# Kernel tuning notes

Hardware: AMD Instinct MI355X
Metric: run time of the kernel (lower is better)

Reference implementation:

```python
import jax, jax.numpy as jnp
import numpy as np

B, C, H, W = 8, 256, 64, 64
IC = 128  # inter_channels = C // reduction


def setup_inputs() -> dict:
    key = jax.random.key(0)
    ks = jax.random.split(key, 9)
    s_in = 1.0 / np.sqrt(C)
    s_ic = 1.0 / np.sqrt(IC)
    return {
        "x": jax.random.normal(ks[0], (B, C, H, W), jnp.float32),
        "wg": jax.random.normal(ks[1], (IC, C), jnp.float32) * s_in,
        "bg": jax.random.normal(ks[2], (IC,), jnp.float32) * s_in,
        "wt": jax.random.normal(ks[3], (IC, C), jnp.float32) * s_in,
        "bt": jax.random.normal(ks[4], (IC,), jnp.float32) * s_in,
        "wp": jax.random.normal(ks[5], (IC, C), jnp.float32) * s_in,
        "bp": jax.random.normal(ks[6], (IC,), jnp.float32) * s_in,
        "wm": jax.random.normal(ks[7], (C, IC), jnp.float32) * s_ic,
        "bm": jax.random.normal(ks[8], (C,), jnp.float32) * s_ic,
    }


def reference(x, wg, bg, wt, bt, wp, bp, wm, bm):
    b, c, h, w = x.shape
    n = h * w
    xf = x.reshape(b, c, n)  # [B, C, N]
    # 1x1 convs are channel matmuls; relu applied after each (as in source)
    g = jax.nn.relu(jnp.einsum('ic,bcn->bni', wg, xf) + bg)          # [B, N, IC]
    theta = jax.nn.relu(jnp.einsum('ic,bcn->bni', wt, xf) + bt)      # [B, N, IC]
    phi = jax.nn.relu(jnp.einsum('ic,bcn->bin', wp, xf) + bp[:, None])  # [B, IC, N]
    scores = jnp.einsum('bni,bim->bnm', theta, phi)                  # [B, N, N] (no scaling)
    attn = jax.nn.softmax(scores, axis=-1)
    out = jnp.einsum('bnm,bmi->bni', attn, g)                        # [B, N, IC]
    mask = jax.nn.relu(jnp.einsum('oc,bnc->bon', wm, out) + bm[None, :, None])
    return mask.reshape(b, c, h, w) + x
```

## Files before the change

kernel.cpp:

```cpp
#include <hip/hip_runtime.h>

typedef __bf16 bf16x8 __attribute__((ext_vector_type(8)));
typedef float f32x4 __attribute__((ext_vector_type(4)));
typedef float f32x16 __attribute__((ext_vector_type(16)));
typedef unsigned short ushort8 __attribute__((ext_vector_type(8)));
typedef unsigned short ushort4v __attribute__((ext_vector_type(4)));
typedef unsigned int uint4v __attribute__((ext_vector_type(4)));

union Frag {
  ushort8 u;
  bf16x8 b;
  uint4v w;
};

__device__ __forceinline__ unsigned short f2bf(float f) {
  unsigned int u = __float_as_uint(f);
  u += 0x7fffu + ((u >> 16) & 1u);
  return (unsigned short)(u >> 16);
}

__device__ __forceinline__ f32x4 fz4() {
  f32x4 v; v[0] = 0.f; v[1] = 0.f; v[2] = 0.f; v[3] = 0.f; return v;
}

__device__ __forceinline__ f32x16 fz16() {
  f32x16 v;
#pragma unroll
  for (int i = 0; i < 16; ++i) v[i] = 0.f;
  return v;
}

#define MFMA16(a, b, c) __builtin_amdgcn_mfma_f32_16x16x32_bf16(a, b, c, 0, 0, 0)
#define MFMA32(a, b, c) __builtin_amdgcn_mfma_f32_32x32x16_bf16(a, b, c, 0, 0, 0)


__global__ void k_prep(const float* __restrict__ wg, const float* __restrict__ wt,
                       const float* __restrict__ wp, const float* __restrict__ wm,
                       unsigned short* __restrict__ wcat, unsigned short* __restrict__ wmb) {
  int t = blockIdx.x * 256 + threadIdx.x;
  if (t < 98304) {
    int o = t >> 8;
    const float* src = (o < 128) ? wt : ((o < 256) ? wp : wg);
    wcat[t] = f2bf(src[(o & 127) * 256 + (t & 255)]);
  }
  if (t < 32768) wmb[t] = f2bf(wm[t]);
}

__device__ __forceinline__ void stage_x(const float* __restrict__ x, int bx, int pt0,
                                        unsigned short* xb, int tid) {
  int c0 = (tid >> 2) * 4;
  int psub = (tid & 3) * 16;
  const float* xbase = x + (size_t)bx * 256 * 4096 + pt0;
  for (int ppc = 0; ppc < 4; ++ppc) {
    int p0 = psub + ppc * 4;
    f32x4 r0 = *(const f32x4*)(xbase + (size_t)(c0 + 0) * 4096 + p0);
    f32x4 r1 = *(const f32x4*)(xbase + (size_t)(c0 + 1) * 4096 + p0);
    f32x4 r2 = *(const f32x4*)(xbase + (size_t)(c0 + 2) * 4096 + p0);
    f32x4 r3 = *(const f32x4*)(xbase + (size_t)(c0 + 3) * 4096 + p0);
    for (int e = 0; e < 4; ++e) {
      ushort4v wv;
      wv[0] = f2bf(r0[e]); wv[1] = f2bf(r1[e]); wv[2] = f2bf(r2[e]); wv[3] = f2bf(r3[e]);
      *(ushort4v*)&xb[(p0 + e) * 264 + c0] = wv;
    }
  }
}

__global__ __launch_bounds__(256, 2) void k_proj_tp(
    const float* __restrict__ x, const unsigned short* __restrict__ wcat,
    const float* __restrict__ bt, const float* __restrict__ bp,
    unsigned short* __restrict__ theta, unsigned short* __restrict__ phiS) {
  __shared__ unsigned short xb[64 * 264];
  int gb = blockIdx.x >> 6;
  size_t ob_off = (size_t)gb * 524288;
  int pt0 = (blockIdx.x & 63) << 6;
  int tid = threadIdx.x;
  stage_x(x, gb, pt0, xb, tid);
  __syncthreads();
  int l = tid & 63, w = tid >> 6, lr = l & 15, lg = l >> 4;
  int obase = w * 64;
  f32x4 acc[4][4];
  for (int i = 0; i < 4; ++i) for (int j = 0; j < 4; ++j) acc[i][j] = fz4();
  for (int kc = 0; kc < 8; ++kc) {
    int ko = kc * 32 + 8 * lg;
    Frag wa[4], xq[4];
    for (int ot = 0; ot < 4; ++ot)
      wa[ot].u = *(const ushort8*)(wcat + (size_t)(obase + ot * 16 + lr) * 256 + ko);
    for (int pt = 0; pt < 4; ++pt)
      xq[pt].u = *(const ushort8*)&xb[(pt * 16 + lr) * 264 + ko];
    for (int ot = 0; ot < 4; ++ot)
      for (int pt = 0; pt < 4; ++pt)
        acc[ot][pt] = MFMA16(wa[ot].b, xq[pt].b, acc[ot][pt]);
  }
  for (int ot = 0; ot < 4; ++ot) {
    int o0 = obase + ot * 16 + 4 * lg;
    float bias[4];
    for (int j = 0; j < 4; ++j) bias[j] = (o0 < 128) ? bt[o0 + j] : bp[o0 + j - 128];
    for (int pt = 0; pt < 4; ++pt) {
      int n = pt0 + pt * 16 + lr;
      ushort4v wv;
      for (int j = 0; j < 4; ++j) {
        float v = acc[ot][pt][j] + bias[j];
        wv[j] = f2bf(v > 0.f ? v : 0.f);
      }
      if (o0 < 128) {
        *(ushort4v*)(theta + ob_off + (size_t)n * 128 + o0) = wv;
      } else {
        int oc = o0 - 128;
        size_t a = (size_t)(n >> 5) * 4096 + (size_t)(oc >> 4) * 512 +
                   (size_t)((oc >> 3) & 1) * 256 + (size_t)(n & 31) * 8 + (oc & 7);
        *(ushort4v*)(phiS + ob_off + a) = wv;
      }
    }
  }
}

__global__ __launch_bounds__(256, 2) void k_proj_g(
    const float* __restrict__ x, const unsigned short* __restrict__ wcat,
    const float* __restrict__ bg, unsigned short* __restrict__ vS) {
  __shared__ unsigned short xb[64 * 264];
  int gb = blockIdx.x >> 6;
  size_t ob_off = (size_t)gb * 524288;
  int pt0 = (blockIdx.x & 63) << 6;
  int tid = threadIdx.x;
  stage_x(x, gb, pt0, xb, tid);
  __syncthreads();
  int l = tid & 63, w = tid >> 6, lr = l & 15, lg = l >> 4;
  f32x4 acc[8];
  for (int i = 0; i < 8; ++i) acc[i] = fz4();
  for (int kc = 0; kc < 8; ++kc) {
    int ko = kc * 32 + 8 * lg;
    Frag xa;
    xa.u = *(const ushort8*)&xb[(w * 16 + lr) * 264 + ko];
    for (int ot = 0; ot < 8; ++ot) {
      Frag wb;
      wb.u = *(const ushort8*)(wcat + (size_t)(256 + ot * 16 + lr) * 256 + ko);
      acc[ot] = MFMA16(xa.b, wb.b, acc[ot]);
    }
  }
  for (int ot = 0; ot < 8; ++ot) {
    int o = ot * 16 + lr;
    float bias = bg[o];
    int n0 = pt0 + w * 16 + 4 * lg;
    ushort4v wv;
    for (int j = 0; j < 4; ++j) {
      float v = acc[ot][j] + bias;
      wv[j] = f2bf(v > 0.f ? v : 0.f);
    }
    size_t a = (size_t)(n0 >> 5) * 4096 +
               (size_t)((o >> 5) * 2 + ((n0 >> 4) & 1)) * 512 +
               (size_t)((((n0 >> 3) & 1) << 5) | (o & 31)) * 8 + (n0 & 7);
    *(ushort4v*)(vS + ob_off + a) = wv;
  }
}

__global__ __launch_bounds__(256, 2) void k_attn(
    const unsigned short* __restrict__ theta, const unsigned short* __restrict__ phiS,
    const unsigned short* __restrict__ vS, unsigned short* __restrict__ out_nm) {
  __shared__ float osum[32][132];
  __shared__ float mls[4][32][2];
  int bid = blockIdx.x;
  int b = bid & 7;
  int q0 = (bid >> 3) << 5;
  int tid = threadIdx.x;
  int l = tid & 63, wid = tid >> 6;
  int ml = l & 31, hi = l >> 5;
  int l8 = l * 8;

  const size_t tbase = ((size_t)b << 12) * 128;
  const unsigned short* pS = phiS + (size_t)b * 524288;
  const unsigned short* vSb = vS + (size_t)b * 524288;

  Frag qf[8];
#pragma unroll
  for (int kc = 0; kc < 8; ++kc)
    qf[kc].u = *(const ushort8*)(theta + tbase +
        (size_t)(q0 + ml) * 128 + kc * 16 + 8 * hi);

  f32x16 oacc[4];
#pragma unroll
  for (int db = 0; db < 4; ++db) oacc[db] = fz16();
  float m = -1e30f, sden = 0.f;

  int t0 = wid * 32;
  Frag pa[8], vt[8];

#pragma unroll
  for (int kc = 0; kc < 8; ++kc)
    pa[kc].u = *(const ushort8*)(pS + (size_t)t0 * 4096 + kc * 512 + l8);

  for (int kt = 0; kt < 32; ++kt) {
    int t = t0 + kt;

    f32x16 sacc = fz16();
#pragma unroll
    for (int kc = 0; kc < 8; ++kc) sacc = MFMA32(pa[kc].b, qf[kc].b, sacc);

#pragma unroll
    for (int t8 = 0; t8 < 8; ++t8)
      vt[t8].u = *(const ushort8*)(vSb + (size_t)t * 4096 + t8 * 512 + l8);

    int tn = t0 + ((kt + 1) & 31);
#pragma unroll
    for (int kc = 0; kc < 8; ++kc)
      pa[kc].u = *(const ushort8*)(pS + (size_t)tn * 4096 + kc * 512 + l8);

    float p[16];
#pragma unroll
    for (int r = 0; r < 16; ++r) p[r] = sacc[r];
    float m8[8];
#pragma unroll
    for (int j = 0; j < 8; ++j) m8[j] = fmaxf(p[j], p[j + 8]);
    float mt = fmaxf(fmaxf(fmaxf(m8[0], m8[1]), fmaxf(m8[2], m8[3])),
                     fmaxf(fmaxf(m8[4], m8[5]), fmaxf(m8[6], m8[7])));
    mt = fmaxf(mt, __shfl_xor(mt, 32));
    if (!__all(mt <= m + 8.0f)) {
      float mn = fmaxf(m, mt);
      float sc = __expf(m - mn);
      sden *= sc;
#pragma unroll
      for (int db = 0; db < 4; ++db) oacc[db] *= sc;
      m = mn;
    }
#pragma unroll
    for (int r = 0; r < 16; ++r) p[r] = __expf(p[r] - m);
    float s8[8];
#pragma unroll
    for (int j = 0; j < 8; ++j) s8[j] = p[j] + p[j + 8];
    float ps = ((s8[0] + s8[1]) + (s8[2] + s8[3])) + ((s8[4] + s8[5]) + (s8[6] + s8[7]));
    ps += __shfl_xor(ps, 32);
    sden += ps;

    unsigned wpk[8], pw[8];
#pragma unroll
    for (int j = 0; j < 8; ++j)
      wpk[j] = (unsigned)f2bf(p[2 * j]) | ((unsigned)f2bf(p[2 * j + 1]) << 16);
#pragma unroll
    for (int j = 0; j < 8; ++j) pw[j] = (unsigned)__shfl_xor((int)wpk[j], 32);
    Frag bf0, bf1;
    bf0.w[0] = hi ? pw[2] : wpk[0];
    bf0.w[1] = hi ? pw[3] : wpk[1];
    bf0.w[2] = hi ? wpk[2] : pw[0];
    bf0.w[3] = hi ? wpk[3] : pw[1];
    bf1.w[0] = hi ? pw[6] : wpk[4];
    bf1.w[1] = hi ? pw[7] : wpk[5];
    bf1.w[2] = hi ? wpk[6] : pw[4];
    bf1.w[3] = hi ? wpk[7] : pw[5];

#pragma unroll
    for (int db = 0; db < 4; ++db) {
      oacc[db] = MFMA32(vt[db * 2].b, bf0.b, oacc[db]);
      oacc[db] = MFMA32(vt[db * 2 + 1].b, bf1.b, oacc[db]);
    }
  }

  if (l < 32) { mls[wid][l][0] = m; mls[wid][l][1] = sden; }
  __syncthreads();
  float M = fmaxf(fmaxf(mls[0][ml][0], mls[1][ml][0]),
                  fmaxf(mls[2][ml][0], mls[3][ml][0]));
  float sc = __expf(m - M);
  for (int w = 0; w < 4; ++w) {
    if (wid == w) {
#pragma unroll
      for (int db = 0; db < 4; ++db)
#pragma unroll
        for (int r = 0; r < 16; ++r) {
          int d = db * 32 + (r & 3) + 8 * (r >> 2) + 4 * hi;
          if (w == 0) osum[ml][d] = oacc[db][r] * sc;
          else        osum[ml][d] += oacc[db][r] * sc;
        }
    }
    __syncthreads();
  }
  {
    int row = wid * 8 + (l >> 3);
    int d0 = (l & 7) * 16;
    float Mx = fmaxf(fmaxf(mls[0][row][0], mls[1][row][0]),
                     fmaxf(mls[2][row][0], mls[3][row][0]));
    float Lt = 0.f;
    for (int w = 0; w < 4; ++w) Lt += mls[w][row][1] * __expf(mls[w][row][0] - Mx);
    float inv = 1.0f / Lt;
    ushort8 w1;
    for (int k = 0; k < 8; ++k) w1[k] = f2bf(osum[row][d0 + k] * inv);
    ushort8 w2;
    for (int k = 0; k < 8; ++k) w2[k] = f2bf(osum[row][d0 + 8 + k] * inv);
    size_t base = tbase + (size_t)(q0 + row) * 128 + d0;
    *(ushort8*)(out_nm + base) = w1;
    *(ushort8*)(out_nm + base + 8) = w2;
  }
}

__global__ __launch_bounds__(256, 2) void k_mask(
    const unsigned short* __restrict__ wmb, const unsigned short* __restrict__ out_nm,
    const float* __restrict__ bm, const float* __restrict__ x,
    float* __restrict__ out) {
  int gb = blockIdx.x >> 6;
  size_t boff = (size_t)gb * 524288;
  int n0 = (blockIdx.x & 63) << 6;
  int tid = threadIdx.x;
  int l = tid & 63, w = tid >> 6, lr = l & 15, lg = l >> 4;
  int ob = w * 64;
  f32x4 acc[4][4];
  for (int i = 0; i < 4; ++i) for (int j = 0; j < 4; ++j) acc[i][j] = fz4();
  for (int kc = 0; kc < 4; ++kc) {
    int ko = kc * 32 + 8 * lg;
    Frag wa[4], xq[4];
    for (int ot = 0; ot < 4; ++ot)
      wa[ot].u = *(const ushort8*)(wmb + (size_t)(ob + ot * 16 + lr) * 128 + ko);
    for (int nt = 0; nt < 4; ++nt)
      xq[nt].u = *(const ushort8*)(out_nm + boff + (size_t)(n0 + nt * 16 + lr) * 128 + ko);
    for (int ot = 0; ot < 4; ++ot)
      for (int nt = 0; nt < 4; ++nt)
        acc[ot][nt] = MFMA16(wa[ot].b, xq[nt].b, acc[ot][nt]);
  }
  for (int ot = 0; ot < 4; ++ot) {
    int o0 = ob + ot * 16 + 4 * lg;
    for (int nt = 0; nt < 4; ++nt) {
      int n = n0 + nt * 16 + lr;
      for (int j = 0; j < 4; ++j) {
        size_t idx = ((size_t)(gb << 8) + o0 + j) * 4096 + n;
        float v = acc[ot][nt][j] + bm[o0 + j];
        v = v > 0.f ? v : 0.f;
        out[idx] = v + x[idx];
      }
    }
  }
}

extern "C" void kernel_launch(void* const* d_in, const int* in_sizes, int n_in,
                              void* d_out, int out_size, void* d_ws, size_t ws_size,
                              hipStream_t stream) {
  const float* x  = (const float*)d_in[0];
  const float* wg = (const float*)d_in[1];
  const float* bg = (const float*)d_in[2];
  const float* wt = (const float*)d_in[3];
  const float* bt = (const float*)d_in[4];
  const float* wp = (const float*)d_in[5];
  const float* bp = (const float*)d_in[6];
  const float* wm = (const float*)d_in[7];
  const float* bm = (const float*)d_in[8];
  float* out = (float*)d_out;

  const size_t SLAB = 524288;
  unsigned short* wcat  = (unsigned short*)d_ws;
  unsigned short* wmb   = wcat + 98304;
  unsigned short* theta = wmb + 32768;
  unsigned short* phiS  = theta + 8 * SLAB;
  unsigned short* vS    = phiS + 8 * SLAB;

  k_prep<<<384, 256, 0, stream>>>(wg, wt, wp, wm, wcat, wmb);
  k_proj_tp<<<512, 256, 0, stream>>>(x, wcat, bt, bp, theta, phiS);
  k_proj_g<<<512, 256, 0, stream>>>(x, wcat, bg, vS);
  k_attn<<<1024, 256, 0, stream>>>(theta, phiS, vS, theta );
  k_mask<<<512, 256, 0, stream>>>(wmb, theta, bm, x, out);
}
```

Measured before the change: 163.7 us.

## Fuse projections, use exp2 softmax, setprio around MFMAs, swizzle attention output

```diff
diff --git a/kernel.cpp b/kernel.cpp
--- a/kernel.cpp
+++ b/kernel.cpp
@@ -32,6 +32,8 @@
 
 #define MFMA16(a, b, c) __builtin_amdgcn_mfma_f32_16x16x32_bf16(a, b, c, 0, 0, 0)
 #define MFMA32(a, b, c) __builtin_amdgcn_mfma_f32_32x32x16_bf16(a, b, c, 0, 0, 0)
+
+#define LOG2E 1.4426950408889634f
 
 
 __global__ void k_prep(const float* __restrict__ wg, const float* __restrict__ wt,
@@ -65,10 +67,12 @@
   }
 }
 
-__global__ __launch_bounds__(256, 2) void k_proj_tp(
+__global__ __launch_bounds__(256, 2) void k_proj(
     const float* __restrict__ x, const unsigned short* __restrict__ wcat,
     const float* __restrict__ bt, const float* __restrict__ bp,
-    unsigned short* __restrict__ theta, unsigned short* __restrict__ phiS) {
+    const float* __restrict__ bg,
+    unsigned short* __restrict__ theta, unsigned short* __restrict__ phiS,
+    unsigned short* __restrict__ vS) {
   __shared__ unsigned short xb[64 * 264];
   int gb = blockIdx.x >> 6;
   size_t ob_off = (size_t)gb * 524288;
@@ -79,7 +83,9 @@
   int l = tid & 63, w = tid >> 6, lr = l & 15, lg = l >> 4;
   int obase = w * 64;
   f32x4 acc[4][4];
+  f32x4 accg[8];
   for (int i = 0; i < 4; ++i) for (int j = 0; j < 4; ++j) acc[i][j] = fz4();
+  for (int i = 0; i < 8; ++i) accg[i] = fz4();
   for (int kc = 0; kc < 8; ++kc) {
     int ko = kc * 32 + 8 * lg;
     Frag wa[4], xq[4];
@@ -90,6 +96,11 @@
     for (int ot = 0; ot < 4; ++ot)
       for (int pt = 0; pt < 4; ++pt)
         acc[ot][pt] = MFMA16(wa[ot].b, xq[pt].b, acc[ot][pt]);
+    for (int ot = 0; ot < 8; ++ot) {
+      Frag wb;
+      wb.u = *(const ushort8*)(wcat + (size_t)(256 + ot * 16 + lr) * 256 + ko);
+      accg[ot] = MFMA16(xq[w].b, wb.b, accg[ot]);
+    }
   }
   for (int ot = 0; ot < 4; ++ot) {
     int o0 = obase + ot * 16 + 4 * lg;
@@ -98,43 +109,22 @@
     for (int pt = 0; pt < 4; ++pt) {
       int n = pt0 + pt * 16 + lr;
       ushort4v wv;
-      for (int j = 0; j < 4; ++j) {
-        float v = acc[ot][pt][j] + bias[j];
-        wv[j] = f2bf(v > 0.f ? v : 0.f);
-      }
       if (o0 < 128) {
+        for (int j = 0; j < 4; ++j) {
+          float v = acc[ot][pt][j] + bias[j];
+          wv[j] = f2bf(v > 0.f ? v * LOG2E : 0.f);
+        }
         *(ushort4v*)(theta + ob_off + (size_t)n * 128 + o0) = wv;
       } else {
+        for (int j = 0; j < 4; ++j) {
+          float v = acc[ot][pt][j] + bias[j];
+          wv[j] = f2bf(v > 0.f ? v : 0.f);
+        }
         int oc = o0 - 128;
         size_t a = (size_t)(n >> 5) * 4096 + (size_t)(oc >> 4) * 512 +
                    (size_t)((oc >> 3) & 1) * 256 + (size_t)(n & 31) * 8 + (oc & 7);
         *(ushort4v*)(phiS + ob_off + a) = wv;
       }
-    }
-  }
-}
-
-__global__ __launch_bounds__(256, 2) void k_proj_g(
-    const float* __restrict__ x, const unsigned short* __restrict__ wcat,
-    const float* __restrict__ bg, unsigned short* __restrict__ vS) {
-  __shared__ unsigned short xb[64 * 264];
-  int gb = blockIdx.x >> 6;
-  size_t ob_off = (size_t)gb * 524288;
-  int pt0 = (blockIdx.x & 63) << 6;
-  int tid = threadIdx.x;
-  stage_x(x, gb, pt0, xb, tid);
-  __syncthreads();
-  int l = tid & 63, w = tid >> 6, lr = l & 15, lg = l >> 4;
-  f32x4 acc[8];
-  for (int i = 0; i < 8; ++i) acc[i] = fz4();
-  for (int kc = 0; kc < 8; ++kc) {
-    int ko = kc * 32 + 8 * lg;
-    Frag xa;
-    xa.u = *(const ushort8*)&xb[(w * 16 + lr) * 264 + ko];
-    for (int ot = 0; ot < 8; ++ot) {
-      Frag wb;
-      wb.u = *(const ushort8*)(wcat + (size_t)(256 + ot * 16 + lr) * 256 + ko);
-      acc[ot] = MFMA16(xa.b, wb.b, acc[ot]);
     }
   }
   for (int ot = 0; ot < 8; ++ot) {
@@ -143,7 +133,7 @@
     int n0 = pt0 + w * 16 + 4 * lg;
     ushort4v wv;
     for (int j = 0; j < 4; ++j) {
-      float v = acc[ot][j] + bias;
+      float v = accg[ot][j] + bias;
       wv[j] = f2bf(v > 0.f ? v : 0.f);
     }
     size_t a = (size_t)(n0 >> 5) * 4096 +
@@ -191,9 +181,11 @@
   for (int kt = 0; kt < 32; ++kt) {
     int t = t0 + kt;
 
+    __builtin_amdgcn_s_setprio(1);
     f32x16 sacc = fz16();
 #pragma unroll
     for (int kc = 0; kc < 8; ++kc) sacc = MFMA32(pa[kc].b, qf[kc].b, sacc);
+    __builtin_amdgcn_s_setprio(0);
 
 #pragma unroll
     for (int t8 = 0; t8 < 8; ++t8)
@@ -204,25 +196,23 @@
     for (int kc = 0; kc < 8; ++kc)
       pa[kc].u = *(const ushort8*)(pS + (size_t)tn * 4096 + kc * 512 + l8);
 
-    float p[16];
-#pragma unroll
-    for (int r = 0; r < 16; ++r) p[r] = sacc[r];
     float m8[8];
 #pragma unroll
-    for (int j = 0; j < 8; ++j) m8[j] = fmaxf(p[j], p[j + 8]);
+    for (int j = 0; j < 8; ++j) m8[j] = fmaxf(sacc[j], sacc[j + 8]);
     float mt = fmaxf(fmaxf(fmaxf(m8[0], m8[1]), fmaxf(m8[2], m8[3])),
                      fmaxf(fmaxf(m8[4], m8[5]), fmaxf(m8[6], m8[7])));
     mt = fmaxf(mt, __shfl_xor(mt, 32));
-    if (!__all(mt <= m + 8.0f)) {
+    if (!__all(mt <= m + 11.5416f)) {
       float mn = fmaxf(m, mt);
-      float sc = __expf(m - mn);
+      float sc = __builtin_exp2f(m - mn);
       sden *= sc;
 #pragma unroll
       for (int db = 0; db < 4; ++db) oacc[db] *= sc;
       m = mn;
     }
-#pragma unroll
-    for (int r = 0; r < 16; ++r) p[r] = __expf(p[r] - m);
+    float p[16];
+#pragma unroll
+    for (int r = 0; r < 16; ++r) p[r] = __builtin_exp2f(sacc[r] - m);
     float s8[8];
 #pragma unroll
     for (int j = 0; j < 8; ++j) s8[j] = p[j] + p[j + 8];
@@ -233,7 +223,7 @@
     unsigned wpk[8], pw[8];
 #pragma unroll
     for (int j = 0; j < 8; ++j)
-      wpk[j] = (unsigned)f2bf(p[2 * j]) | ((unsigned)f2bf(p[2 * j + 1]) << 16);
+      asm("v_cvt_pk_bf16_f32 %0, %1, %2" : "=v"(wpk[j]) : "v"(p[2 * j]), "v"(p[2 * j + 1]));
 #pragma unroll
     for (int j = 0; j < 8; ++j) pw[j] = (unsigned)__shfl_xor((int)wpk[j], 32);
     Frag bf0, bf1;
@@ -246,18 +236,20 @@
     bf1.w[2] = hi ? wpk[6] : pw[4];
     bf1.w[3] = hi ? wpk[7] : pw[5];
 
+    __builtin_amdgcn_s_setprio(1);
 #pragma unroll
     for (int db = 0; db < 4; ++db) {
       oacc[db] = MFMA32(vt[db * 2].b, bf0.b, oacc[db]);
       oacc[db] = MFMA32(vt[db * 2 + 1].b, bf1.b, oacc[db]);
     }
+    __builtin_amdgcn_s_setprio(0);
   }
 
   if (l < 32) { mls[wid][l][0] = m; mls[wid][l][1] = sden; }
   __syncthreads();
   float M = fmaxf(fmaxf(mls[0][ml][0], mls[1][ml][0]),
                   fmaxf(mls[2][ml][0], mls[3][ml][0]));
-  float sc = __expf(m - M);
+  float sc = __builtin_exp2f(m - M);
   for (int w = 0; w < 4; ++w) {
     if (wid == w) {
 #pragma unroll
@@ -277,15 +269,16 @@
     float Mx = fmaxf(fmaxf(mls[0][row][0], mls[1][row][0]),
                      fmaxf(mls[2][row][0], mls[3][row][0]));
     float Lt = 0.f;
-    for (int w = 0; w < 4; ++w) Lt += mls[w][row][1] * __expf(mls[w][row][0] - Mx);
+    for (int w = 0; w < 4; ++w) Lt += mls[w][row][1] * __builtin_exp2f(mls[w][row][0] - Mx);
     float inv = 1.0f / Lt;
     ushort8 w1;
     for (int k = 0; k < 8; ++k) w1[k] = f2bf(osum[row][d0 + k] * inv);
     ushort8 w2;
     for (int k = 0; k < 8; ++k) w2[k] = f2bf(osum[row][d0 + 8 + k] * inv);
-    size_t base = tbase + (size_t)(q0 + row) * 128 + d0;
-    *(ushort8*)(out_nm + base) = w1;
-    *(ushort8*)(out_nm + base + 8) = w2;
+    size_t a = (size_t)b * 524288 + (size_t)(q0 >> 5) * 4096 +
+               (size_t)(d0 >> 4) * 512 + (size_t)row * 8;
+    *(ushort8*)(out_nm + a) = w1;
+    *(ushort8*)(out_nm + a + 256) = w2;
   }
 }
 
@@ -303,11 +296,16 @@
   for (int i = 0; i < 4; ++i) for (int j = 0; j < 4; ++j) acc[i][j] = fz4();
   for (int kc = 0; kc < 4; ++kc) {
     int ko = kc * 32 + 8 * lg;
+    int kc2 = kc * 2 + (lg >> 1), hi2 = lg & 1;
     Frag wa[4], xq[4];
     for (int ot = 0; ot < 4; ++ot)
       wa[ot].u = *(const ushort8*)(wmb + (size_t)(ob + ot * 16 + lr) * 128 + ko);
-    for (int nt = 0; nt < 4; ++nt)
-      xq[nt].u = *(const ushort8*)(out_nm + boff + (size_t)(n0 + nt * 16 + lr) * 128 + ko);
+    for (int nt = 0; nt < 4; ++nt) {
+      int t = (n0 >> 5) + (nt >> 1);
+      int mln = ((nt & 1) << 4) + lr;
+      xq[nt].u = *(const ushort8*)(out_nm + boff + (size_t)t * 4096 +
+                                   (size_t)kc2 * 512 + (size_t)(hi2 * 32 + mln) * 8);
+    }
     for (int ot = 0; ot < 4; ++ot)
       for (int nt = 0; nt < 4; ++nt)
         acc[ot][nt] = MFMA16(wa[ot].b, xq[nt].b, acc[ot][nt]);
@@ -348,8 +346,7 @@
   unsigned short* vS    = phiS + 8 * SLAB;
 
   k_prep<<<384, 256, 0, stream>>>(wg, wt, wp, wm, wcat, wmb);
-  k_proj_tp<<<512, 256, 0, stream>>>(x, wcat, bt, bp, theta, phiS);
-  k_proj_g<<<512, 256, 0, stream>>>(x, wcat, bg, vS);
+  k_proj<<<512, 256, 0, stream>>>(x, wcat, bt, bp, bg, theta, phiS, vS);
   k_attn<<<1024, 256, 0, stream>>>(theta, phiS, vS, theta );
   k_mask<<<512, 256, 0, stream>>>(wmb, theta, bm, x, out);
 }
```

After: 167.8 us. 2.5% more time.
